# Performance work log

Measured on AMD Instinct MI355X. Metric: run time of the kernel, lower is better.

## Reference

```python
import jax, jax.numpy as jnp
import numpy as np

D_MODEL = 1024
N_HEADS = 16
D_HEAD = D_MODEL // N_HEADS
NEG_INF = -1000000000.0


def setup_inputs() -> dict:
    key = jax.random.key(0)
    ks = jax.random.split(key, 12)
    B, S1, S2 = 2, 2048, 2048
    query = jax.random.normal(ks[0], (B, S1, D_MODEL), dtype=jnp.float32)
    k_in = jax.random.normal(ks[1], (B, S2, D_MODEL), dtype=jnp.float32)
    v_in = jax.random.normal(ks[2], (B, S2, D_MODEL), dtype=jnp.float32)
    # causal mask: True = position is masked out (filled with -1e9)
    mask = jnp.broadcast_to(jnp.triu(jnp.ones((S1, S2), dtype=bool), k=1), (B, S1, S2))
    s = 1.0 / np.sqrt(D_MODEL)
    W_q = jax.random.uniform(ks[3], (D_MODEL, D_MODEL), jnp.float32, -s, s)
    b_q = jax.random.uniform(ks[4], (D_MODEL,), jnp.float32, -s, s)
    W_k = jax.random.uniform(ks[5], (D_MODEL, D_MODEL), jnp.float32, -s, s)
    b_k = jax.random.uniform(ks[6], (D_MODEL,), jnp.float32, -s, s)
    W_v = jax.random.uniform(ks[7], (D_MODEL, D_MODEL), jnp.float32, -s, s)
    b_v = jax.random.uniform(ks[8], (D_MODEL,), jnp.float32, -s, s)
    W_o = jax.random.uniform(ks[9], (D_MODEL, D_MODEL), jnp.float32, -s, s)
    b_o = jax.random.uniform(ks[10], (D_MODEL,), jnp.float32, -s, s)
    return {"query": query, "key": k_in, "value": v_in, "mask": mask,
            "W_q": W_q, "b_q": b_q, "W_k": W_k, "b_k": b_k,
            "W_v": W_v, "b_v": b_v, "W_o": W_o, "b_o": b_o}


def reference(query, key, value, mask, W_q, b_q, W_k, b_k, W_v, b_v, W_o, b_o):
    B, S1, _ = query.shape
    S2 = key.shape[1]
    scalar = 1.0 / np.sqrt(D_HEAD)
    # projections (torch Linear: x @ W.T + b)
    Q = (query @ W_q.T + b_q).reshape(B, S1, N_HEADS, D_HEAD).transpose(0, 2, 1, 3)
    K = (key @ W_k.T + b_k).reshape(B, S2, N_HEADS, D_HEAD).transpose(0, 2, 1, 3)
    V = (value @ W_v.T + b_v).reshape(B, S2, N_HEADS, D_HEAD).transpose(0, 2, 1, 3)
    # [B, H, S1, S2]
    scores = jnp.einsum('bhqd,bhkd->bhqk', Q, K) * scalar
    scores = jnp.where(mask[:, None, :, :], NEG_INF, scores)
    probs = jax.nn.softmax(scores, axis=-1)
    attn = jnp.einsum('bhqk,bhkd->bhqd', probs, V)
    concat = attn.transpose(0, 2, 1, 3).reshape(B, S1, D_MODEL)
    return concat @ W_o.T + b_o
```

## Files before the change

### kernel.cpp

```cpp
#include <hip/hip_runtime.h>
#include <hip/hip_bf16.h>
#include <stdint.h>

typedef __bf16 bf16;
typedef __bf16 bf16x8 __attribute__((ext_vector_type(8)));
typedef float f32x4 __attribute__((ext_vector_type(4)));
typedef float f32x16 __attribute__((ext_vector_type(16)));
typedef unsigned int u32;
typedef u32 u32x4 __attribute__((ext_vector_type(4)));

#define D_MODEL 1024
#define S_LEN 2048
#define NB 2
#define NH 16
#define DH 64

__device__ __forceinline__ void gload_lds16(const bf16* g, bf16* l) {
    auto gp = reinterpret_cast<const __attribute__((address_space(1))) unsigned int*>(
        reinterpret_cast<uintptr_t>(g));
    auto lp = reinterpret_cast<__attribute__((address_space(3))) unsigned int*>(
        reinterpret_cast<uintptr_t>(l));
    __builtin_amdgcn_global_load_lds(gp, lp, 16, 0, 0);
}

__device__ __forceinline__ u32 cvtpk(float lo, float hi) {
    u32 r; asm("v_cvt_pk_bf16_f32 %0, %1, %2" : "=v"(r) : "v"(lo), "v"(hi)); return r;
}
__device__ __forceinline__ void plswap(u32& a, u32& b) {
    asm("v_permlane32_swap_b32 %0, %1" : "+v"(a), "+v"(b));
}

__global__ __launch_bounds__(256)
void cvt_all(const float* __restrict__ q, const float* __restrict__ k,
             const float* __restrict__ v, const float* __restrict__ w0,
             const float* __restrict__ w1, const float* __restrict__ w2,
             const float* __restrict__ w3,
             bf16* __restrict__ oq, bf16* __restrict__ ok, bf16* __restrict__ ov,
             bf16* __restrict__ o0, bf16* __restrict__ o1, bf16* __restrict__ o2,
             bf16* __restrict__ o3)
{
    const int bid = blockIdx.x;
    const float* in; bf16* out; int local;
    if (bid < 6144) {
        int r = bid >> 11; local = bid & 2047;
        in  = (r == 0) ? q  : (r == 1) ? k  : v;
        out = (r == 0) ? oq : (r == 1) ? ok : ov;
    } else {
        int wb = bid - 6144;
        int r = wb >> 9; local = wb & 511;
        in  = (r == 0) ? w0 : (r == 1) ? w1 : (r == 2) ? w2 : w3;
        out = (r == 0) ? o0 : (r == 1) ? o1 : (r == 2) ? o2 : o3;
    }
    const size_t i = ((size_t)local * 256 + threadIdx.x) * 8;
    f32x4 x = *(const f32x4*)(in + i);
    f32x4 y = *(const f32x4*)(in + i + 4);
    bf16x8 o;
    #pragma unroll
    for (int j = 0; j < 4; ++j) { o[j] = (bf16)x[j]; o[4 + j] = (bf16)y[j]; }
    *(bf16x8*)(out + i) = o;
}

__global__ __launch_bounds__(256, 2)
void gemm_qkv2(const bf16* __restrict__ Aq, const bf16* __restrict__ Ak, const bf16* __restrict__ Av,
               const bf16* __restrict__ Wq, const bf16* __restrict__ Wk, const bf16* __restrict__ Wv,
               const float* __restrict__ bq, const float* __restrict__ bk, const float* __restrict__ bv,
               bf16* __restrict__ QPo, bf16* __restrict__ KPo, bf16* __restrict__ VPo, float qscale)
{
    __shared__ __align__(16) char gsm[34816];
    bf16* As = (bf16*)gsm;
    bf16* Bs = (bf16*)(gsm + 16384);

    const int K = 1024;
    const int t = threadIdx.x, lane = t & 63, wid = t >> 6;
    const int nbn = 24;
    const int cpx = gridDim.x >> 3;
    const int bid = blockIdx.x;
    const int swz = (bid & 7) * cpx + (bid >> 3);
    const int bm0 = (swz / nbn) << 7;
    const int bn0 = (swz % nbn) << 7;
    const int sel = bn0 >> 10;
    const int nl  = bn0 & 1023;
    const bf16* Ap = (sel == 0) ? Aq : (sel == 1) ? Ak : Av;
    const bf16* Bp = (sel == 0) ? Wq : (sel == 1) ? Wk : Wv;
    const float* bias = (sel == 0) ? bq : (sel == 1) ? bk : bv;

    const int r16 = lane & 15, g = lane >> 4;
    const int wr = (wid >> 1) << 6;
    const int wc = (wid & 1) << 6;

    f32x4 acc[4][4] = {};

    const int sch = t;

    for (int k0 = 0; k0 < K; k0 += 64) {
        #pragma unroll
        for (int i = 0; i < 4; ++i) {
            int ch = wid * 256 + i * 64 + lane;
            int row = ch >> 3, c8 = ch & 7;
            int sc = c8 ^ (row & 7);
            gload_lds16(Ap + (size_t)(bm0 + row) * K + k0 + sc * 8, As + ch * 8);
            gload_lds16(Bp + (size_t)(nl + row) * K + k0 + sc * 8, Bs + ch * 8);
        }
        __syncthreads();
        #pragma unroll
        for (int ks = 0; ks < 2; ++ks) {
            const int cl = ks * 4 + g;
            bf16x8 af[4], bfr[4];
            #pragma unroll
            for (int mi = 0; mi < 4; ++mi) {
                int row = wr + mi * 16 + r16;
                af[mi] = *(const bf16x8*)((const char*)As + row * 128 + ((cl ^ (row & 7)) << 4));
            }
            #pragma unroll
            for (int ni = 0; ni < 4; ++ni) {
                int row = wc + ni * 16 + r16;
                bfr[ni] = *(const bf16x8*)((const char*)Bs + row * 128 + ((cl ^ (row & 7)) << 4));
            }
            #pragma unroll
            for (int mi = 0; mi < 4; ++mi)
                #pragma unroll
                for (int ni = 0; ni < 4; ++ni)
                    acc[mi][ni] = __builtin_amdgcn_mfma_f32_16x16x32_bf16(af[mi], bfr[ni], acc[mi][ni], 0, 0, 0);
        }
        __syncthreads();
    }
    (void)sch;

    const int rb = g * 4;
    const int b2 = bm0 >> 11, kt0 = (bm0 & 2047) >> 5;
    if (sel != 2) {
        const float cs = (sel == 0) ? qscale : 1.0f;
        bf16* dst = (sel == 0) ? QPo : KPo;
        bf16* Ts = (bf16*)gsm;
        #pragma unroll
        for (int mi = 0; mi < 4; ++mi)
            #pragma unroll
            for (int ni = 0; ni < 4; ++ni) {
                int dl = wc + ni * 16 + r16;
                float bv = bias[nl + dl];
                #pragma unroll
                for (int r = 0; r < 4; ++r) {
                    int sl = wr + mi * 16 + rb + r;
                    Ts[sl * 136 + dl] = (bf16)((acc[mi][ni][r] + bv) * cs);
                }
            }
        __syncthreads();
        #pragma unroll
        for (int i2 = 0; i2 < 8; ++i2) {
            int ch = t + i2 * 256;
            int hloc = ch >> 10, rem = ch & 1023;
            int kt32loc = rem >> 8, db = (rem >> 6) & 3, ln = rem & 63;
            int srcs = kt32loc * 32 + (ln & 31);
            int srcd = hloc * 64 + db * 16 + (ln >> 5) * 8;
            bf16x8 v = *(const bf16x8*)&Ts[srcs * 136 + srcd];
            int bh2 = b2 * 16 + (nl >> 6) + hloc;
            int kt32 = kt0 + kt32loc;
            *(bf16x8*)(dst + (((size_t)(bh2 * 64 + kt32) * 4 + db) * 64 + ln) * 8) = v;
        }
    } else {
        bf16* Ts = (bf16*)gsm;
        #pragma unroll
        for (int mi = 0; mi < 4; ++mi)
            #pragma unroll
            for (int ni = 0; ni < 4; ++ni) {
                int dl = wc + ni * 16 + r16;
                float bv = bias[nl + dl];
                #pragma unroll
                for (int r = 0; r < 4; ++r) {
                    int sl = wr + mi * 16 + rb + r;
                    Ts[dl * 136 + sl] = (bf16)(acc[mi][ni][r] + bv);
                }
            }
        __syncthreads();
        #pragma unroll
        for (int i2 = 0; i2 < 8; ++i2) {
            int ch = t + i2 * 256;
            int hloc = ch >> 10, rem = ch & 1023;
            int kt32loc = rem >> 8, kb = (rem >> 7) & 1, dt = (rem >> 6) & 1, ln = rem & 63;
            int srcd = hloc * 64 + dt * 32 + (ln & 31);
            int srcs = kt32loc * 32 + kb * 16 + (ln >> 5) * 8;
            bf16x8 v = *(const bf16x8*)&Ts[srcd * 136 + srcs];
            int bh2 = b2 * 16 + (nl >> 6) + hloc;
            int kt32 = kt0 + kt32loc;
            *(bf16x8*)(VPo + ((((size_t)(bh2 * 64 + kt32) * 2 + kb) * 2 + dt) * 64 + ln) * 8) = v;
        }
    }
}

__global__ __launch_bounds__(256)
void gemm_out(const bf16* __restrict__ Ap, const bf16* __restrict__ Bp,
              const float* __restrict__ bias, float* __restrict__ Cp)
{
    __shared__ __align__(16) bf16 As[128 * 64];
    __shared__ __align__(16) bf16 Bs[64 * 64];

    const int K = 1024, N = 1024;
    const int t = threadIdx.x, lane = t & 63, wid = t >> 6;
    const int nbn = 16;
    const int cpx = gridDim.x >> 3;
    const int bid = blockIdx.x;
    const int swz = (bid & 7) * cpx + (bid >> 3);
    const int bm0 = (swz / nbn) << 7;
    const int bn0 = (swz % nbn) << 6;
    const int r16 = lane & 15, g = lane >> 4;
    const int wr = (wid >> 1) << 6;
    const int wc = (wid & 1) << 5;

    f32x4 acc[4][2] = {};

    for (int k0 = 0; k0 < K; k0 += 64) {
        #pragma unroll
        for (int i = 0; i < 4; ++i) {
            int ch = wid * 256 + i * 64 + lane;
            int row = ch >> 3, c8 = ch & 7;
            int sc = c8 ^ (row & 7);
            gload_lds16(Ap + (size_t)(bm0 + row) * K + k0 + sc * 8, &As[ch * 8]);
        }
        #pragma unroll
        for (int i = 0; i < 2; ++i) {
            int ch = wid * 128 + i * 64 + lane;
            int row = ch >> 3, c8 = ch & 7;
            int sc = c8 ^ (row & 7);
            gload_lds16(Bp + (size_t)(bn0 + row) * K + k0 + sc * 8, &Bs[ch * 8]);
        }
        __syncthreads();
        #pragma unroll
        for (int ks = 0; ks < 2; ++ks) {
            const int cl = ks * 4 + g;
            bf16x8 af[4], bfr[2];
            #pragma unroll
            for (int mi = 0; mi < 4; ++mi) {
                int row = wr + mi * 16 + r16;
                af[mi] = *(const bf16x8*)((const char*)&As[0] + row * 128 + ((cl ^ (row & 7)) << 4));
            }
            #pragma unroll
            for (int ni = 0; ni < 2; ++ni) {
                int row = wc + ni * 16 + r16;
                bfr[ni] = *(const bf16x8*)((const char*)&Bs[0] + row * 128 + ((cl ^ (row & 7)) << 4));
            }
            #pragma unroll
            for (int mi = 0; mi < 4; ++mi)
                #pragma unroll
                for (int ni = 0; ni < 2; ++ni)
                    acc[mi][ni] = __builtin_amdgcn_mfma_f32_16x16x32_bf16(af[mi], bfr[ni], acc[mi][ni], 0, 0, 0);
        }
        __syncthreads();
    }

    const int rb = g * 4;
    #pragma unroll
    for (int mi = 0; mi < 4; ++mi) {
        #pragma unroll
        for (int ni = 0; ni < 2; ++ni) {
            int cg = bn0 + wc + ni * 16 + r16;
            float bv = bias[cg];
            #pragma unroll
            for (int r = 0; r < 4; ++r) {
                int rg = bm0 + wr + mi * 16 + rb + r;
                Cp[(size_t)rg * N + cg] = acc[mi][ni][r] + bv;
            }
        }
    }
}

__global__ __launch_bounds__(256, 2)
void attn11(const bf16* __restrict__ QP, const bf16* __restrict__ KP,
            const bf16* __restrict__ VP, bf16* __restrict__ Ob)
{
    __shared__ float Of[4][64][33];
    __shared__ float lS[4][32];

    const int t = threadIdx.x, lane = t & 63, wv = t >> 6;
    const int l31 = lane & 31, hh = lane >> 5;

    const int bid = blockIdx.x;
    const int xcd = bid & 7, s = bid >> 3;
    const int bh = xcd * 4 + (s & 3);
    const int jp = s >> 2;
    const int b = bh >> 4, h = bh & 15;

    const bf16* kp0 = KP + (size_t)bh * 131072 + lane * 8;
    const bf16* vp0 = VP + (size_t)bh * 131072 + lane * 8;

    #pragma unroll 1
    for (int ph = 0; ph < 2; ++ph) {
        const int J = ph ? (63 - jp) : jp;
        const int n = J + 1;
        const int r0 = (wv * n) >> 2;
        const int r1 = ((wv + 1) * n) >> 2;

        f32x16 oacc[2] = {};
        float lsum = 0.f;

        if (r0 < r1) {
            bf16x8 qf[4];
            {
                const bf16* qp = QP + ((size_t)(bh * 64 + J) * 4) * 512 + lane * 8;
                #pragma unroll
                for (int db = 0; db < 4; ++db) qf[db] = *(const bf16x8*)(qp + db * 512);
            }

            auto loadK = [&](int tt, bf16x8 (&kf)[4]) {
                const bf16* p = kp0 + (size_t)tt * 2048;
                #pragma unroll
                for (int db = 0; db < 4; ++db) kf[db] = *(const bf16x8*)(p + db * 512);
            };
            auto loadV = [&](int tt, bf16x8 (&vf)[4]) {
                const bf16* p = vp0 + (size_t)tt * 2048;
                #pragma unroll
                for (int q2 = 0; q2 < 4; ++q2) vf[q2] = *(const bf16x8*)(p + q2 * 512);
            };

            auto process = [&](const bf16x8 (&kf)[4], const bf16x8 (&vf)[4], bool diag) {
                f32x16 sacc = {};
                __builtin_amdgcn_s_setprio(1);
                #pragma unroll
                for (int db = 0; db < 4; ++db)
                    sacc = __builtin_amdgcn_mfma_f32_32x32x16_bf16(kf[db], qf[db], sacc, 0, 0, 0);
                __builtin_amdgcn_s_setprio(0);
                if (diag) {
                    #pragma unroll
                    for (int r2 = 0; r2 < 16; ++r2) {
                        int cr = (r2 & 3) + 8 * (r2 >> 2) + 4 * hh;
                        if (cr > l31) sacc[r2] = -1e9f;
                    }
                }
                #pragma unroll
                for (int r2 = 0; r2 < 16; ++r2) {
                    float p = __builtin_exp2f(sacc[r2]);
                    sacc[r2] = p;
                    lsum += p;
                }
                #pragma unroll
                for (int kb = 0; kb < 2; ++kb) {
                    u32 w0 = cvtpk(sacc[kb * 8 + 0], sacc[kb * 8 + 1]);
                    u32 w2 = cvtpk(sacc[kb * 8 + 4], sacc[kb * 8 + 5]);
                    u32 w1 = cvtpk(sacc[kb * 8 + 2], sacc[kb * 8 + 3]);
                    u32 w3 = cvtpk(sacc[kb * 8 + 6], sacc[kb * 8 + 7]);
                    plswap(w0, w2);
                    plswap(w1, w3);
                    u32x4 pw; pw[0] = w0; pw[1] = w1; pw[2] = w2; pw[3] = w3;
                    bf16x8 pb = __builtin_bit_cast(bf16x8, pw);
                    __builtin_amdgcn_s_setprio(1);
                    #pragma unroll
                    for (int dt = 0; dt < 2; ++dt)
                        oacc[dt] = __builtin_amdgcn_mfma_f32_32x32x16_bf16(vf[kb * 2 + dt], pb, oacc[dt], 0, 0, 0);
                    __builtin_amdgcn_s_setprio(0);
                }
            };

            bf16x8 kfA[4], kfB[4], vfA[4], vfB[4];
            loadK(r0, kfA); loadV(r0, vfA);
            int r = r0;
            for (;;) {
                if (r + 1 < r1) { loadK(r + 1, kfB); loadV(r + 1, vfB); }
                process(kfA, vfA, r == J);
                if (++r >= r1) break;
                if (r + 1 < r1) { loadK(r + 1, kfA); loadV(r + 1, vfA); }
                process(kfB, vfB, r == J);
                if (++r >= r1) break;
            }
        }

        lsum += __shfl_xor(lsum, 32);

        #pragma unroll
        for (int dt = 0; dt < 2; ++dt)
            #pragma unroll
            for (int r2 = 0; r2 < 16; ++r2) {
                int d = dt * 32 + (r2 & 3) + 8 * (r2 >> 2) + 4 * hh;
                Of[wv][d][l31] = oacc[dt][r2];
            }
        if (hh == 0) lS[wv][l31] = lsum;
        __syncthreads();

        {
            const int q = t >> 3, c8 = t & 7;
            float l = lS[0][q] + lS[1][q] + lS[2][q] + lS[3][q];
            float inv = 1.0f / l;
            bf16x8 o8;
            #pragma unroll
            for (int i = 0; i < 8; ++i) {
                int d = c8 * 8 + i;
                float o = Of[0][d][q] + Of[1][d][q] + Of[2][d][q] + Of[3][d][q];
                o8[i] = (bf16)(o * inv);
            }
            *(bf16x8*)(Ob + ((size_t)(b * S_LEN + J * 32 + q)) * D_MODEL + h * DH + c8 * 8) = o8;
        }
        __syncthreads();
    }
}

extern "C" void kernel_launch(void* const* d_in, const int* in_sizes, int n_in,
                              void* d_out, int out_size, void* d_ws, size_t ws_size,
                              hipStream_t stream)
{
    const float* query = (const float*)d_in[0];
    const float* key   = (const float*)d_in[1];
    const float* value = (const float*)d_in[2];
    const float* W_q = (const float*)d_in[4];
    const float* b_q = (const float*)d_in[5];
    const float* W_k = (const float*)d_in[6];
    const float* b_k = (const float*)d_in[7];
    const float* W_v = (const float*)d_in[8];
    const float* b_v = (const float*)d_in[9];
    const float* W_o = (const float*)d_in[10];
    const float* b_o = (const float*)d_in[11];

    char* w = (char*)d_ws;
    const size_t MB = 1 << 20;
    bf16* qbf = (bf16*)(w);
    bf16* kbf = (bf16*)(w + 8 * MB);
    bf16* vbf = (bf16*)(w + 16 * MB);
    bf16* QP  = (bf16*)(w + 24 * MB);
    bf16* KP  = (bf16*)(w + 32 * MB);
    bf16* VP  = (bf16*)(w + 40 * MB);
    bf16* Wqb = (bf16*)(w + 48 * MB);
    bf16* Wkb = (bf16*)(w + 50 * MB);
    bf16* Wvb = (bf16*)(w + 52 * MB);
    bf16* Wob = (bf16*)(w + 54 * MB);
    bf16* Ob  = (bf16*)(w);

    dim3 blk(256);
    cvt_all<<<dim3(8192), blk, 0, stream>>>(query, key, value, W_q, W_k, W_v, W_o,
                                            qbf, kbf, vbf, Wqb, Wkb, Wvb, Wob);

    const float qscale = 0.125f * 1.4426950408889634f;
    gemm_qkv2<<<dim3(768), blk, 0, stream>>>(qbf, kbf, vbf, Wqb, Wkb, Wvb,
                                             b_q, b_k, b_v, QP, KP, VP, qscale);

    attn11<<<dim3(1024), blk, 0, stream>>>(QP, KP, VP, Ob);

    gemm_out<<<dim3(512), blk, 0, stream>>>(Ob, Wob, b_o, (float*)d_out);
}
```

Baseline: 99.33 us.

## Software-pipeline QK MFMA of next tile with softmax of current tile

Splits the attention inner-loop body into a QK score step and a finish step. The QK MFMA for tile r+1 is now issued before the exp/PV work of tile r, and the K/V loads for tile r+2 are placed between those stages, so matrix work can overlap with transcendental and VALU work. It also replaces the serial row-sum accumulation with a pairwise tree sum to shorten the dependency chain. The cost is an extra 16-float accumulator held live, which raises register pressure under the 2-blocks-per-CU launch bound.

```diff
diff --git a/kernel.cpp b/kernel.cpp
--- a/kernel.cpp
+++ b/kernel.cpp
@@ -90,8 +90,6 @@
 
     f32x4 acc[4][4] = {};
 
-    const int sch = t;
-
     for (int k0 = 0; k0 < K; k0 += 64) {
         #pragma unroll
         for (int i = 0; i < 4; ++i) {
@@ -124,7 +122,6 @@
         }
         __syncthreads();
     }
-    (void)sch;
 
     const int rb = g * 4;
     const int b2 = bm0 >> 11, kt0 = (bm0 & 2047) >> 5;
@@ -264,7 +261,7 @@
 }
 
 __global__ __launch_bounds__(256, 2)
-void attn11(const bf16* __restrict__ QP, const bf16* __restrict__ KP,
+void attn12(const bf16* __restrict__ QP, const bf16* __restrict__ KP,
             const bf16* __restrict__ VP, bf16* __restrict__ Ob)
 {
     __shared__ float Of[4][64][33];
@@ -310,14 +307,16 @@
                 #pragma unroll
                 for (int q2 = 0; q2 < 4; ++q2) vf[q2] = *(const bf16x8*)(p + q2 * 512);
             };
-
-            auto process = [&](const bf16x8 (&kf)[4], const bf16x8 (&vf)[4], bool diag) {
+            auto qk = [&](const bf16x8 (&kf)[4]) -> f32x16 {
                 f32x16 sacc = {};
                 __builtin_amdgcn_s_setprio(1);
                 #pragma unroll
                 for (int db = 0; db < 4; ++db)
                     sacc = __builtin_amdgcn_mfma_f32_32x32x16_bf16(kf[db], qf[db], sacc, 0, 0, 0);
                 __builtin_amdgcn_s_setprio(0);
+                return sacc;
+            };
+            auto finish = [&](f32x16& sacc, const bf16x8 (&vf)[4], bool diag) {
                 if (diag) {
                     #pragma unroll
                     for (int r2 = 0; r2 < 16; ++r2) {
@@ -326,10 +325,15 @@
                     }
                 }
                 #pragma unroll
-                for (int r2 = 0; r2 < 16; ++r2) {
-                    float p = __builtin_exp2f(sacc[r2]);
-                    sacc[r2] = p;
-                    lsum += p;
+                for (int r2 = 0; r2 < 16; ++r2)
+                    sacc[r2] = __builtin_exp2f(sacc[r2]);
+                {
+                    float s0 = sacc[0] + sacc[1],   s1 = sacc[2] + sacc[3];
+                    float s2 = sacc[4] + sacc[5],   s3 = sacc[6] + sacc[7];
+                    float s4 = sacc[8] + sacc[9],   s5 = sacc[10] + sacc[11];
+                    float s6 = sacc[12] + sacc[13], s7 = sacc[14] + sacc[15];
+                    float t0 = s0 + s1, t1 = s2 + s3, t2 = s4 + s5, t3 = s6 + s7;
+                    lsum += (t0 + t1) + (t2 + t3);
                 }
                 #pragma unroll
                 for (int kb = 0; kb < 2; ++kb) {
@@ -349,15 +353,22 @@
                 }
             };
 
-            bf16x8 kfA[4], kfB[4], vfA[4], vfB[4];
+            bf16x8 kfA[4], vfA[4], kfB[4], vfB[4];
+            f32x16 saccA, saccB;
             loadK(r0, kfA); loadV(r0, vfA);
+            if (r0 + 1 < r1) { loadK(r0 + 1, kfB); loadV(r0 + 1, vfB); }
+            saccA = qk(kfA);
             int r = r0;
             for (;;) {
-                if (r + 1 < r1) { loadK(r + 1, kfB); loadV(r + 1, vfB); }
-                process(kfA, vfA, r == J);
+                if (r + 1 < r1) saccB = qk(kfB);
+                if (r + 2 < r1) loadK(r + 2, kfA);
+                finish(saccA, vfA, r == J);
+                if (r + 2 < r1) loadV(r + 2, vfA);
                 if (++r >= r1) break;
-                if (r + 1 < r1) { loadK(r + 1, kfA); loadV(r + 1, vfA); }
-                process(kfB, vfB, r == J);
+                if (r + 1 < r1) saccA = qk(kfA);
+                if (r + 2 < r1) loadK(r + 2, kfB);
+                finish(saccB, vfB, r == J);
+                if (r + 2 < r1) loadV(r + 2, vfB);
                 if (++r >= r1) break;
             }
         }
@@ -429,7 +440,7 @@
     gemm_qkv2<<<dim3(768), blk, 0, stream>>>(qbf, kbf, vbf, Wqb, Wkb, Wvb,
                                              b_q, b_k, b_v, QP, KP, VP, qscale);
 
-    attn11<<<dim3(1024), blk, 0, stream>>>(QP, KP, VP, Ob);
+    attn12<<<dim3(1024), blk, 0, stream>>>(QP, KP, VP, Ob);
 
     gemm_out<<<dim3(512), blk, 0, stream>>>(Ob, Wob, b_o, (float*)d_out);
 }
```

Result: no change. 99.81 us (+0.5%).
